# Performance work log

Measured on AMD Instinct MI355X. Metric: run time of the kernel, lower is better.

Reference implementation:

```python
import jax, jax.numpy as jnp
import numpy as np

B, N, D = 8, 2048, 256
K = 16384  # codebook_size


def setup_inputs() -> dict:
    key = jax.random.key(0)
    k1, k2, k3, k4 = jax.random.split(key, 4)
    z = jax.random.normal(k1, (B, N, D), dtype=jnp.float32)
    emb_weight = jax.random.normal(k2, (K, D), dtype=jnp.float32) * 0.02
    proj_w = jax.random.normal(k3, (D, D), dtype=jnp.float32) * (1.0 / np.sqrt(D))
    proj_b = jax.random.normal(k4, (D,), dtype=jnp.float32) * 0.01
    return {"z": z, "emb_weight": emb_weight, "proj_w": proj_w, "proj_b": proj_b}


def reference(z, emb_weight, proj_w, proj_b):
    # emb = embedding_proj(embedding.weight)  (torch Linear: x @ W^T + b)
    emb = emb_weight @ proj_w.T + proj_b  # (K, D)
    b, n, d = z.shape
    zf = z.reshape(b * n, d)  # (BN, D)
    # squared euclidean distances: ||z||^2 + ||e||^2 - 2 z e^T
    dist = (
        jnp.sum(zf * zf, axis=1, keepdims=True)
        + jnp.sum(emb * emb, axis=1)
        - 2.0 * jnp.einsum("bd,kd->bk", zf, emb)
    )  # (BN, K)
    q_indices = jnp.argmin(dist, axis=1)  # (BN,) int
    quantized = emb[q_indices].reshape(z.shape)  # (B, N, D)
    # straight-through estimator
    quantized = z + jax.lax.stop_gradient(quantized - z)
    q_indices = q_indices.reshape(b, n)
    # (unregularized_z, emb, regularized_z, bottleneck_rep)
    return z, emb, quantized, q_indices
```

## Files before the change

### kernel.cpp

```cpp
#include <hip/hip_runtime.h>
#include <hip/hip_bf16.h>

#define D       256
#define KCB     16384
#define BNROWS  16384
#define NT      4
#define MARGIN  0.15f
#define ZMAX    5.0f
#define EMAX    0.2f
#define FS2U    (2.0f * (ZMAX / 127.0f) * (EMAX / 127.0f))
#define MARGIN_INT 1210u
#define IBIAS   8388608

typedef __attribute__((ext_vector_type(4))) int   int4v;
typedef __attribute__((ext_vector_type(4))) float f32x4;
typedef unsigned long long u64;

__device__ __forceinline__ void gload_lds16(const void* g, void* l) {
    __builtin_amdgcn_global_load_lds(
        (const __attribute__((address_space(1))) void*)g,
        (__attribute__((address_space(3))) void*)l, 16, 0, 0);
}

__device__ __forceinline__ unsigned fmap(float f) {
    unsigned u = __float_as_uint(f);
    return (u & 0x80000000u) ? ~u : (u | 0x80000000u);
}

__device__ __forceinline__ signed char q8(float x, float s) {
    return (signed char)__float2int_rn(fminf(fmaxf(x * s, -127.f), 127.f));
}

__global__ __launch_bounds__(256) void prep_kernel(
    const float* __restrict__ z, signed char* __restrict__ z8,
    const float* __restrict__ ew, const float* __restrict__ pw,
    const float* __restrict__ pb, float* __restrict__ emb,
    signed char* __restrict__ e8)
{
    __shared__ float Et[64][65];
    __shared__ float Pt[64][65];
    const int tid = threadIdx.x;

    if (blockIdx.x < 4096) {
        const int i = blockIdx.x * 256 + tid;
        float4 v = ((const float4*)z)[i];
        const float s = 127.0f / ZMAX;
        char4 c;
        c.x = q8(v.x, s); c.y = q8(v.y, s); c.z = q8(v.z, s); c.w = q8(v.w, s);
        ((char4*)z8)[i] = c;
        return;
    }

    const int bid = blockIdx.x - 4096;
    const int tc  = tid & 15, tr = tid >> 4;
    const int k0  = (bid >> 2) * 64;
    const int d0  = (bid & 3) * 64;

    float acc[4][4];
#pragma unroll
    for (int a = 0; a < 4; ++a)
#pragma unroll
        for (int b = 0; b < 4; ++b) acc[a][b] = 0.f;

    for (int j0 = 0; j0 < 256; j0 += 64) {
        __syncthreads();
#pragma unroll
        for (int i = 0; i < 4; ++i) {
            const int c = i * 256 + tid;
            const int r = c >> 4, c4 = (c & 15) * 4;
            float4 v = *(const float4*)(ew + (size_t)(k0 + r) * 256 + j0 + c4);
            Et[r][c4 + 0] = v.x; Et[r][c4 + 1] = v.y;
            Et[r][c4 + 2] = v.z; Et[r][c4 + 3] = v.w;
            float4 w = *(const float4*)(pw + (size_t)(d0 + r) * 256 + j0 + c4);
            Pt[r][c4 + 0] = w.x; Pt[r][c4 + 1] = w.y;
            Pt[r][c4 + 2] = w.z; Pt[r][c4 + 3] = w.w;
        }
        __syncthreads();
        for (int j = 0; j < 64; ++j) {
            float ev[4], pv[4];
#pragma unroll
            for (int a = 0; a < 4; ++a) ev[a] = Et[tr * 4 + a][j];
#pragma unroll
            for (int b = 0; b < 4; ++b) pv[b] = Pt[tc * 4 + b][j];
#pragma unroll
            for (int a = 0; a < 4; ++a)
#pragma unroll
                for (int b = 0; b < 4; ++b)
                    acc[a][b] = fmaf(ev[a], pv[b], acc[a][b]);
        }
    }

    const float4 bias = *(const float4*)(pb + d0 + tc * 4);
    const float se = 127.0f / EMAX;
#pragma unroll
    for (int a = 0; a < 4; ++a) {
        float4 o;
        o.x = acc[a][0] + bias.x; o.y = acc[a][1] + bias.y;
        o.z = acc[a][2] + bias.z; o.w = acc[a][3] + bias.w;
        const size_t off = (size_t)(k0 + tr * 4 + a) * 256 + d0 + tc * 4;
        *(float4*)(emb + off) = o;
        char4 c;
        c.x = q8(o.x, se); c.y = q8(o.y, se);
        c.z = q8(o.z, se); c.w = q8(o.w, se);
        *(char4*)(e8 + off) = c;
    }
}

__global__ __launch_bounds__(256) void snorm_kernel(
    const float* __restrict__ emb, float* __restrict__ s,
    int* __restrict__ s_bi)
{
    const int tid = threadIdx.x;
    const int row = blockIdx.x * 64 + (tid >> 2);
    const int qd  = tid & 3;
    const size_t base = (size_t)row * 256;
    float sq = 0.f;
#pragma unroll
    for (int j = 0; j < 16; ++j) {
        const int off = qd * 4 + j * 16;
        float4 v = *(const float4*)(emb + base + off);
        sq = fmaf(v.x, v.x, fmaf(v.y, v.y, fmaf(v.z, v.z, fmaf(v.w, v.w, sq))));
    }
    sq += __shfl_xor(sq, 1);
    sq += __shfl_xor(sq, 2);
    if (qd == 0) {
        s[row]    = sq;
        s_bi[row] = (int)rintf(sq / FS2U) + IBIAS;
    }
}

__global__ __launch_bounds__(512, 4) void argmin_hi_kernel(
    const signed char* __restrict__ z8, const signed char* __restrict__ e8,
    const int* __restrict__ s_bi,
    unsigned* __restrict__ partial1, unsigned* __restrict__ partial2)
{
    __shared__ alignas(16) short A_lds[3 * 4096];
    __shared__ alignas(16) short B_lds[3 * 8192];

    const int tid  = threadIdx.x;
    const int lane = tid & 63;
    const int wid  = tid >> 6;
    const int wz   = wid >> 2;
    const int wc   = wid & 3;
    const int lcol = lane & 15;
    const int rhi  = lane >> 4;

    const int bm = blockIdx.x >> 6;
    const int bn = blockIdx.x & 63;
    const size_t r0 = (size_t)bm * 128;
    const size_t n0 = (size_t)bn * 256;

    const int slot  = (((lcol & 1) * 4 + rhi) ^ ((lcol >> 1) & 7)) << 3;
    const int aoff0 = wz * 2048 + (lcol >> 1) * 64 + slot;
    const int boff0 = wc * 2048 + (lcol >> 1) * 64 + slot;

    auto goff = [](int c) {
        const int l = c >> 3, u = (c & 7) ^ (l & 7);
        return (size_t)(2 * l + (u >> 2)) * 256 + (size_t)(u & 3) * 16;
    };
    const size_t gA  = goff(tid);
    const int    cB0 = wid * 128 + lane;
    const int    cB1 = cB0 + 64;
    const size_t gB0 = goff(cB0);
    const size_t gB1 = goff(cB1);

    short* const aDst  = A_lds + tid * 8;
    short* const bDst0 = B_lds + cB0 * 8;
    short* const bDst1 = B_lds + cB1 * 8;

    const char* const z8B = (const char*)z8 + r0 * 256;
    const char* const e8B = (const char*)e8 + n0 * 256;

    gload_lds16(z8B + gA, aDst);
    gload_lds16(e8B + gB0, bDst0);
    gload_lds16(e8B + gB1, bDst1);
    gload_lds16(z8B + 64 + gA, aDst + 4096);
    gload_lds16(e8B + 64 + gB0, bDst0 + 8192);
    gload_lds16(e8B + 64 + gB1, bDst1 + 8192);
    asm volatile("s_waitcnt vmcnt(3)" ::: "memory");
    __builtin_amdgcn_s_barrier();

    int4v acc[4][4];
    const int4v izero = {0, 0, 0, 0};
#pragma unroll
    for (int m = 0; m < 4; ++m)
#pragma unroll
        for (int n = 0; n < 4; ++n) acc[m][n] = izero;

#define TILE_BODY(JL)                                                         \
    {                                                                         \
        const int t  = i3 + (JL);                                             \
        const int tp = t + 2;                                                 \
        int4v bq[4];                                                          \
        _Pragma("unroll")                                                     \
        for (int n = 0; n < 4; ++n)            \
            bq[n] = *(const int4v*)(A_lds + (JL) * 4096 + aoff0 + n * 512);   \
        if (tp < NT) {                                                        \
            const char* Ab = z8B + ((size_t)tp << 6);                         \
            const char* Bb = e8B + ((size_t)tp << 6);                         \
            gload_lds16(Ab + gA, aDst + (((JL) + 2) % 3) * 4096);             \
            gload_lds16(Bb + gB0, bDst0 + (((JL) + 2) % 3) * 8192);           \
            gload_lds16(Bb + gB1, bDst1 + (((JL) + 2) % 3) * 8192);           \
        }                                                                     \
        __builtin_amdgcn_s_setprio(1);                                        \
        _Pragma("unroll")                                                     \
        for (int m = 0; m < 4; ++m) {       \
            const int4v am = *(const int4v*)(B_lds + (JL) * 8192 + boff0 + m * 512); \
            _Pragma("unroll")                                                 \
            for (int n = 0; n < 4; ++n)                                       \
                acc[m][n] = __builtin_amdgcn_mfma_i32_16x16x64_i8(            \
                    am, bq[n], acc[m][n], 0, 0, 0);                           \
        }                                                                     \
        __builtin_amdgcn_s_setprio(0);                                        \
        if (tp < NT)                                                          \
            asm volatile("s_waitcnt vmcnt(3)" ::: "memory");                  \
        else if (t + 1 < NT)                                                  \
            asm volatile("s_waitcnt vmcnt(0)" ::: "memory");                  \
        __builtin_amdgcn_s_barrier();                                         \
    }

    {
        const int i3 = 0;
        TILE_BODY(0)
        TILE_BODY(1)
        TILE_BODY(2)
    }
    {
        const int i3 = 3;
        TILE_BODY(0)
    }
#undef TILE_BODY

    int4v sb[4];
#pragma unroll
    for (int mc = 0; mc < 4; ++mc)
        sb[mc] = *(const int4v*)(s_bi + n0 + wc * 64 + mc * 16 + rhi * 4);

    u64* cand = (u64*)A_lds;
#pragma unroll
    for (int nz = 0; nz < 4; ++nz) {
        unsigned v[16];
#pragma unroll
        for (int mc = 0; mc < 4; ++mc) {
            const unsigned cb = (unsigned)(wc * 64 + mc * 16 + rhi * 4);
#pragma unroll
            for (int j = 0; j < 4; ++j)
                v[mc * 4 + j] =
                    ((unsigned)(sb[mc][j] - acc[mc][nz][j]) << 8) | (cb + j);
        }
        unsigned p1 = min(v[0], v[1]), p2 = max(v[0], v[1]);
#pragma unroll
        for (int i = 1; i < 8; ++i) {
            const unsigned l = min(v[2 * i], v[2 * i + 1]);
            const unsigned h = max(v[2 * i], v[2 * i + 1]);
            const unsigned t = max(p1, l);
            p1 = min(p1, l);
            p2 = min(t, min(p2, h));
        }
#pragma unroll
        for (int mask = 16; mask <= 32; mask <<= 1) {
            const unsigned q1 = __shfl_xor(p1, mask);
            const unsigned q2 = __shfl_xor(p2, mask);
            const unsigned t  = max(p1, q1);
            p1 = min(p1, q1);
            p2 = min(t, min(p2, q2));
        }
        if (rhi == 0) {
            const int row = wz * 64 + nz * 16 + lcol;
            cand[row * 4 + wc] = (u64)p1 | ((u64)p2 << 32);
        }
    }
    __syncthreads();
    if (tid < 128) {
        const u64* c4 = cand + (size_t)tid * 4;
        u64 a = c4[0];
        unsigned p1 = (unsigned)a, p2 = (unsigned)(a >> 32);
#pragma unroll
        for (int w = 1; w < 4; ++w) {
            a = c4[w];
            const unsigned q1 = (unsigned)a, q2 = (unsigned)(a >> 32);
            const unsigned t  = max(p1, q1);
            p1 = min(p1, q1);
            p2 = min(t, min(p2, q2));
        }
        partial1[(size_t)bn * BNROWS + r0 + tid] = p1;
        partial2[(size_t)bn * BNROWS + r0 + tid] = p2;
    }
}

__global__ __launch_bounds__(256) void collect_rescore_kernel(
    const unsigned* __restrict__ partial1, const unsigned* __restrict__ partial2,
    const float* __restrict__ z, const float* __restrict__ emb,
    const float* __restrict__ s,
    float* __restrict__ outz, float* __restrict__ outq,
    float* __restrict__ outidx)
{
    __shared__ unsigned gsb;
    __shared__ int      nsel;
    __shared__ int      selk[128];
    __shared__ u64      wbest[4];
    __shared__ int      kfin;

    const int tid  = threadIdx.x;
    const int row  = blockIdx.x;
    const int lane = tid & 63;
    const int wid  = tid >> 6;

    unsigned v = 0xFFFFFFFFu;
    int vbn = 0;
    if (tid < 64)       { v = partial1[(size_t)tid * BNROWS + row];        vbn = tid; }
    else if (tid < 128) { v = partial2[(size_t)(tid - 64) * BNROWS + row]; vbn = tid - 64; }

    if (tid < 64) {
        unsigned g = v;
#pragma unroll
        for (int mm = 1; mm < 64; mm <<= 1) g = min(g, (unsigned)__shfl_xor(g, mm));
        if (tid == 0) { gsb = g; nsel = 0; }
    }
    __syncthreads();

    const unsigned thr = (((gsb >> 8) + MARGIN_INT) << 8) | 0xFFu;
    if (tid < 128 && v <= thr) {
        const int i = atomicAdd(&nsel, 1);
        selk[i] = vbn * 256 + (int)(v & 0xFFu);
    }
    __syncthreads();

    const float4 zv = *(const float4*)(z + (size_t)row * 256 + lane * 4);
    const int ns = nsel;
    u64 best = ~0ull;
    for (int i = wid; i < ns; i += 4) {
        const int k = selk[i];
        const float4 ev = *(const float4*)(emb + (size_t)k * 256 + lane * 4);
        float p = zv.x * ev.x;
        p = fmaf(zv.y, ev.y, p);
        p = fmaf(zv.z, ev.z, p);
        p = fmaf(zv.w, ev.w, p);
#pragma unroll
        for (int mm = 1; mm < 64; mm <<= 1) p += __shfl_xor(p, mm);
        const float sc = fmaf(-2.f, p, s[k]);
        const u64 pk = ((u64)fmap(sc) << 32) | (unsigned)k;
        best = (pk < best) ? pk : best;
    }
    if (lane == 0) wbest[wid] = best;
    __syncthreads();
    if (tid == 0) {
        u64 b = wbest[0];
        if (wbest[1] < b) b = wbest[1];
        if (wbest[2] < b) b = wbest[2];
        if (wbest[3] < b) b = wbest[3];
        kfin = (int)(b & 0xffffffffu);
        outidx[row] = (float)kfin;
    }
    __syncthreads();

    const int k = kfin;
    outz[(size_t)row * 256 + tid] = z[(size_t)row * 256 + tid];
    outq[(size_t)row * 256 + tid] = emb[(size_t)k * 256 + tid];
}

extern "C" void kernel_launch(void* const* d_in, const int* in_sizes, int n_in,
                              void* d_out, int out_size, void* d_ws, size_t ws_size,
                              hipStream_t stream)
{
    const float* z  = (const float*)d_in[0];
    const float* ew = (const float*)d_in[1];
    const float* pw = (const float*)d_in[2];
    const float* pb = (const float*)d_in[3];

    float* out     = (float*)d_out;
    float* out_z   = out;
    float* out_emb = out + (size_t)BNROWS * D;
    float* out_q   = out + 2 * (size_t)BNROWS * D;
    float* out_idx = out + 3 * (size_t)BNROWS * D;

    float*       sbuf  = (float*)d_ws;
    int*         s_bi  = (int*)((char*)d_ws + 65536);
    signed char* z8    = (signed char*)((char*)d_ws + 131072);
    unsigned*    part1 = (unsigned*)((char*)d_ws + 131072 + 4194304);
    unsigned*    part2 = (unsigned*)((char*)d_ws + 131072 + 2 * 4194304);
    signed char* e8    = (signed char*)out_q;

    prep_kernel<<<4096 + 1024, 256, 0, stream>>>(z, z8, ew, pw, pb, out_emb, e8);
    snorm_kernel<<<KCB / 64, 256, 0, stream>>>(out_emb, sbuf, s_bi);
    argmin_hi_kernel<<<(BNROWS / 128) * (KCB / 256), 512, 0, stream>>>(
        z8, e8, s_bi, part1, part2);
    collect_rescore_kernel<<<BNROWS, 256, 0, stream>>>(
        part1, part2, z, out_emb, sbuf, out_z, out_q, out_idx);
}
```

Measured before the change: 180.0 us.

## Make argmin kernel persistent with codebook tile resident in LDS

Launches 512 persistent blocks instead of 8192. Each block keeps its 256-entry int8 codebook slice (all four K-steps) resident in LDS and loops over 16 row tiles, streaming only the z tiles through a double buffer. This removes the repeated reloading of codebook tiles and the per-block launch and prologue cost. In exchange the z-tile loads are only one step ahead and wait on vmcnt(0) each step. LDS per block grows and the grid is smaller, so overlap and occupancy may drop.

```diff
diff --git a/kernel.cpp b/kernel.cpp
--- a/kernel.cpp
+++ b/kernel.cpp
@@ -4,7 +4,6 @@
 #define D       256
 #define KCB     16384
 #define BNROWS  16384
-#define NT      4
 #define MARGIN  0.15f
 #define ZMAX    5.0f
 #define EMAX    0.2f
@@ -134,8 +133,8 @@
     const int* __restrict__ s_bi,
     unsigned* __restrict__ partial1, unsigned* __restrict__ partial2)
 {
-    __shared__ alignas(16) short A_lds[3 * 4096];
-    __shared__ alignas(16) short B_lds[3 * 8192];
+    __shared__ alignas(16) short A_lds[2 * 4096];
+    __shared__ alignas(16) short B_lds[4 * 8192];
 
     const int tid  = threadIdx.x;
     const int lane = tid & 63;
@@ -145,9 +144,8 @@
     const int lcol = lane & 15;
     const int rhi  = lane >> 4;
 
-    const int bm = blockIdx.x >> 6;
-    const int bn = blockIdx.x & 63;
-    const size_t r0 = (size_t)bm * 128;
+    const int bn  = blockIdx.x & 63;
+    const int bm0 = blockIdx.x >> 6;
     const size_t n0 = (size_t)bn * 256;
 
     const int slot  = (((lcol & 1) * 4 + rhi) ^ ((lcol >> 1) & 7)) << 3;
@@ -164,128 +162,128 @@
     const size_t gB0 = goff(cB0);
     const size_t gB1 = goff(cB1);
 
-    short* const aDst  = A_lds + tid * 8;
-    short* const bDst0 = B_lds + cB0 * 8;
-    short* const bDst1 = B_lds + cB1 * 8;
-
-    const char* const z8B = (const char*)z8 + r0 * 256;
     const char* const e8B = (const char*)e8 + n0 * 256;
-
-    gload_lds16(z8B + gA, aDst);
-    gload_lds16(e8B + gB0, bDst0);
-    gload_lds16(e8B + gB1, bDst1);
-    gload_lds16(z8B + 64 + gA, aDst + 4096);
-    gload_lds16(e8B + 64 + gB0, bDst0 + 8192);
-    gload_lds16(e8B + 64 + gB1, bDst1 + 8192);
-    asm volatile("s_waitcnt vmcnt(3)" ::: "memory");
+    const char*       zc  = (const char*)z8 + (size_t)bm0 * 32768;
+
+#pragma unroll
+    for (int t = 0; t < 4; ++t) {
+        gload_lds16(e8B + (t << 6) + gB0, (void*)(B_lds + t * 8192 + cB0 * 8));
+        gload_lds16(e8B + (t << 6) + gB1, (void*)(B_lds + t * 8192 + cB1 * 8));
+    }
+    gload_lds16(zc + gA,      (void*)(A_lds + tid * 8));
+    gload_lds16(zc + 64 + gA, (void*)(A_lds + 4096 + tid * 8));
+    asm volatile("s_waitcnt vmcnt(1)" ::: "memory");
     __builtin_amdgcn_s_barrier();
 
-    int4v acc[4][4];
-    const int4v izero = {0, 0, 0, 0};
-#pragma unroll
-    for (int m = 0; m < 4; ++m)
-#pragma unroll
-        for (int n = 0; n < 4; ++n) acc[m][n] = izero;
-
-#define TILE_BODY(JL)                                                         \
+#define COMPUTE_TILE(ABUF, BT)                                                \
     {                                                                         \
-        const int t  = i3 + (JL);                                             \
-        const int tp = t + 2;                                                 \
         int4v bq[4];                                                          \
         _Pragma("unroll")                                                     \
-        for (int n = 0; n < 4; ++n)            \
-            bq[n] = *(const int4v*)(A_lds + (JL) * 4096 + aoff0 + n * 512);   \
-        if (tp < NT) {                                                        \
-            const char* Ab = z8B + ((size_t)tp << 6);                         \
-            const char* Bb = e8B + ((size_t)tp << 6);                         \
-            gload_lds16(Ab + gA, aDst + (((JL) + 2) % 3) * 4096);             \
-            gload_lds16(Bb + gB0, bDst0 + (((JL) + 2) % 3) * 8192);           \
-            gload_lds16(Bb + gB1, bDst1 + (((JL) + 2) % 3) * 8192);           \
-        }                                                                     \
+        for (int n = 0; n < 4; ++n)                                           \
+            bq[n] = *(const int4v*)(A_lds + (ABUF) * 4096 + aoff0 + n * 512); \
         __builtin_amdgcn_s_setprio(1);                                        \
         _Pragma("unroll")                                                     \
-        for (int m = 0; m < 4; ++m) {       \
-            const int4v am = *(const int4v*)(B_lds + (JL) * 8192 + boff0 + m * 512); \
+        for (int m = 0; m < 4; ++m) {                                         \
+            const int4v am = *(const int4v*)(B_lds + (BT) * 8192 + boff0 + m * 512); \
             _Pragma("unroll")                                                 \
             for (int n = 0; n < 4; ++n)                                       \
                 acc[m][n] = __builtin_amdgcn_mfma_i32_16x16x64_i8(            \
                     am, bq[n], acc[m][n], 0, 0, 0);                           \
         }                                                                     \
         __builtin_amdgcn_s_setprio(0);                                        \
-        if (tp < NT)                                                          \
-            asm volatile("s_waitcnt vmcnt(3)" ::: "memory");                  \
-        else if (t + 1 < NT)                                                  \
-            asm volatile("s_waitcnt vmcnt(0)" ::: "memory");                  \
-        __builtin_amdgcn_s_barrier();                                         \
-    }
-
-    {
-        const int i3 = 0;
-        TILE_BODY(0)
-        TILE_BODY(1)
-        TILE_BODY(2)
-    }
-    {
-        const int i3 = 3;
-        TILE_BODY(0)
-    }
-#undef TILE_BODY
-
-    int4v sb[4];
-#pragma unroll
-    for (int mc = 0; mc < 4; ++mc)
-        sb[mc] = *(const int4v*)(s_bi + n0 + wc * 64 + mc * 16 + rhi * 4);
-
-    u64* cand = (u64*)A_lds;
-#pragma unroll
-    for (int nz = 0; nz < 4; ++nz) {
-        unsigned v[16];
-#pragma unroll
-        for (int mc = 0; mc < 4; ++mc) {
-            const unsigned cb = (unsigned)(wc * 64 + mc * 16 + rhi * 4);
-#pragma unroll
-            for (int j = 0; j < 4; ++j)
-                v[mc * 4 + j] =
-                    ((unsigned)(sb[mc][j] - acc[mc][nz][j]) << 8) | (cb + j);
+    }
+
+#pragma unroll 1
+    for (int i = 0; i < 16; ++i) {
+        const bool more = (i < 15);
+
+        int4v acc[4][4];
+        const int4v izero = {0, 0, 0, 0};
+#pragma unroll
+        for (int m = 0; m < 4; ++m)
+#pragma unroll
+            for (int n = 0; n < 4; ++n) acc[m][n] = izero;
+
+        COMPUTE_TILE(0, 0)
+        asm volatile("s_waitcnt vmcnt(0)" ::: "memory");
+        __builtin_amdgcn_s_barrier();
+
+        gload_lds16(zc + 128 + gA, (void*)(A_lds + tid * 8));
+        COMPUTE_TILE(1, 1)
+        asm volatile("s_waitcnt vmcnt(0)" ::: "memory");
+        __builtin_amdgcn_s_barrier();
+
+        gload_lds16(zc + 192 + gA, (void*)(A_lds + 4096 + tid * 8));
+        COMPUTE_TILE(0, 2)
+        asm volatile("s_waitcnt vmcnt(0)" ::: "memory");
+        __builtin_amdgcn_s_barrier();
+
+        if (more) gload_lds16(zc + 262144 + gA, (void*)(A_lds + tid * 8));
+        COMPUTE_TILE(1, 3)
+        __builtin_amdgcn_s_barrier();
+
+        int4v sb[4];
+#pragma unroll
+        for (int mc = 0; mc < 4; ++mc)
+            sb[mc] = *(const int4v*)(s_bi + n0 + wc * 64 + mc * 16 + rhi * 4);
+
+        u64* cand = (u64*)(A_lds + 4096);
+#pragma unroll
+        for (int nz = 0; nz < 4; ++nz) {
+            unsigned v[16];
+#pragma unroll
+            for (int mc = 0; mc < 4; ++mc) {
+                const unsigned cb = (unsigned)(wc * 64 + mc * 16 + rhi * 4);
+#pragma unroll
+                for (int j = 0; j < 4; ++j)
+                    v[mc * 4 + j] =
+                        ((unsigned)(sb[mc][j] - acc[mc][nz][j]) << 8) | (cb + j);
+            }
+            unsigned p1 = min(v[0], v[1]), p2 = max(v[0], v[1]);
+#pragma unroll
+            for (int q = 1; q < 8; ++q) {
+                const unsigned l = min(v[2 * q], v[2 * q + 1]);
+                const unsigned h = max(v[2 * q], v[2 * q + 1]);
+                const unsigned t = max(p1, l);
+                p1 = min(p1, l);
+                p2 = min(t, min(p2, h));
+            }
+#pragma unroll
+            for (int mask = 16; mask <= 32; mask <<= 1) {
+                const unsigned q1 = __shfl_xor(p1, mask);
+                const unsigned q2 = __shfl_xor(p2, mask);
+                const unsigned t  = max(p1, q1);
+                p1 = min(p1, q1);
+                p2 = min(t, min(p2, q2));
+            }
+            if (rhi == 0) {
+                const int row = wz * 64 + nz * 16 + lcol;
+                cand[row * 4 + wc] = (u64)p1 | ((u64)p2 << 32);
+            }
         }
-        unsigned p1 = min(v[0], v[1]), p2 = max(v[0], v[1]);
-#pragma unroll
-        for (int i = 1; i < 8; ++i) {
-            const unsigned l = min(v[2 * i], v[2 * i + 1]);
-            const unsigned h = max(v[2 * i], v[2 * i + 1]);
-            const unsigned t = max(p1, l);
-            p1 = min(p1, l);
-            p2 = min(t, min(p2, h));
+        __syncthreads();
+        if (tid < 128) {
+            const u64* c4 = cand + (size_t)tid * 4;
+            u64 a = c4[0];
+            unsigned p1 = (unsigned)a, p2 = (unsigned)(a >> 32);
+#pragma unroll
+            for (int w = 1; w < 4; ++w) {
+                a = c4[w];
+                const unsigned q1 = (unsigned)a, q2 = (unsigned)(a >> 32);
+                const unsigned t  = max(p1, q1);
+                p1 = min(p1, q1);
+                p2 = min(t, min(p2, q2));
+            }
+            const size_t r0 = (size_t)(bm0 + 8 * i) * 128;
+            partial1[(size_t)bn * BNROWS + r0 + tid] = p1;
+            partial2[(size_t)bn * BNROWS + r0 + tid] = p2;
         }
-#pragma unroll
-        for (int mask = 16; mask <= 32; mask <<= 1) {
-            const unsigned q1 = __shfl_xor(p1, mask);
-            const unsigned q2 = __shfl_xor(p2, mask);
-            const unsigned t  = max(p1, q1);
-            p1 = min(p1, q1);
-            p2 = min(t, min(p2, q2));
-        }
-        if (rhi == 0) {
-            const int row = wz * 64 + nz * 16 + lcol;
-            cand[row * 4 + wc] = (u64)p1 | ((u64)p2 << 32);
-        }
-    }
-    __syncthreads();
-    if (tid < 128) {
-        const u64* c4 = cand + (size_t)tid * 4;
-        u64 a = c4[0];
-        unsigned p1 = (unsigned)a, p2 = (unsigned)(a >> 32);
-#pragma unroll
-        for (int w = 1; w < 4; ++w) {
-            a = c4[w];
-            const unsigned q1 = (unsigned)a, q2 = (unsigned)(a >> 32);
-            const unsigned t  = max(p1, q1);
-            p1 = min(p1, q1);
-            p2 = min(t, min(p2, q2));
-        }
-        partial1[(size_t)bn * BNROWS + r0 + tid] = p1;
-        partial2[(size_t)bn * BNROWS + r0 + tid] = p2;
-    }
+        __syncthreads();
+
+        if (more) gload_lds16(zc + 262144 + 64 + gA, (void*)(A_lds + 4096 + tid * 8));
+        zc += 262144;
+    }
+#undef COMPUTE_TILE
 }
 
 __global__ __launch_bounds__(256) void collect_rescore_kernel(
@@ -383,8 +381,7 @@
 
     prep_kernel<<<4096 + 1024, 256, 0, stream>>>(z, z8, ew, pw, pb, out_emb, e8);
     snorm_kernel<<<KCB / 64, 256, 0, stream>>>(out_emb, sbuf, s_bi);
-    argmin_hi_kernel<<<(BNROWS / 128) * (KCB / 256), 512, 0, stream>>>(
-        z8, e8, s_bi, part1, part2);
+    argmin_hi_kernel<<<512, 512, 0, stream>>>(z8, e8, s_bi, part1, part2);
     collect_rescore_kernel<<<BNROWS, 256, 0, stream>>>(
         part1, part2, z, out_emb, sbuf, out_z, out_q, out_idx);
 }
```

Result: no change. 177.4 us (median of 2 runs) (-1.4%).
